# Optimization experiments

Measured on AMD Instinct MI355X. Metric: run time of the kernel, lower is better.

The kernel has to match this reference:

```python
import jax, jax.numpy as jnp
import numpy as np
import math

B, S, D, H = 8, 1024, 1024, 16
DH = D // H  # 64


def setup_inputs() -> dict:
    key = jax.random.key(0)
    ks = jax.random.split(key, 10)
    inputs = jax.random.normal(ks[0], (B, S, D), dtype=jnp.float32)
    mask = jax.random.randint(ks[1], (B, S, S), 0, 2) == 1  # bool [B,S,S]
    sc = 1.0 / math.sqrt(D)
    # per-head projection weights stacked: [H, D, DH], biases [H, DH]
    Wq = jax.random.normal(ks[2], (H, D, DH), dtype=jnp.float32) * sc
    bq = jax.random.normal(ks[3], (H, DH), dtype=jnp.float32) * 0.02
    Wk = jax.random.normal(ks[4], (H, D, DH), dtype=jnp.float32) * sc
    bk = jax.random.normal(ks[5], (H, DH), dtype=jnp.float32) * 0.02
    Wv = jax.random.normal(ks[6], (H, D, DH), dtype=jnp.float32) * sc
    bv = jax.random.normal(ks[7], (H, DH), dtype=jnp.float32) * 0.02
    Wo = jax.random.normal(ks[8], (D, D), dtype=jnp.float32) * sc
    bo = jax.random.normal(ks[9], (D,), dtype=jnp.float32) * 0.02
    return {"inputs": inputs, "mask": mask, "Wq": Wq, "bq": bq, "Wk": Wk,
            "bk": bk, "Wv": Wv, "bv": bv, "Wo": Wo, "bo": bo}


def reference(inputs, mask, Wq, bq, Wk, bk, Wv, bv, Wo, bo):
    d_model = inputs.shape[-1]
    scale = 1.0 / jnp.sqrt(jnp.asarray(d_model, inputs.dtype))  # note: sqrt(d_model), as in source
    # batched per-head projections: [B,H,S,DH]
    Q = jnp.einsum('bsd,hde->bhse', inputs, Wq) + bq[None, :, None, :]
    K = jnp.einsum('bsd,hde->bhse', inputs, Wk) + bk[None, :, None, :]
    V = jnp.einsum('bsd,hde->bhse', inputs, Wv) + bv[None, :, None, :]
    scores = jnp.einsum('bhse,bhte->bhst', Q, K) * scale  # [B,H,S,S]
    scores = jnp.where(mask[:, None, :, :], jnp.asarray(-1e9, scores.dtype), scores)
    attn = jax.nn.softmax(scores, axis=-1)
    ctx = jnp.einsum('bhst,bhte->bhse', attn, V)  # [B,H,S,DH]
    # concat heads along last dim (head h -> slice h*DH:(h+1)*DH), matches torch.cat
    bsz, h, s, dh = ctx.shape
    x = ctx.transpose(0, 2, 1, 3).reshape(bsz, s, h * dh)
    return x @ Wo + bo
```

## Files before the change

kernel.cpp:

```cpp
#include <hip/hip_runtime.h>
#include <hip/hip_bf16.h>
#include <stdint.h>


typedef __attribute__((ext_vector_type(8))) short short8;
typedef __attribute__((ext_vector_type(4))) float floatx4;

__device__ __forceinline__ int swz(int r, int kc) { return r * 8 + (kc ^ (r & 7)); }
__device__ __forceinline__ short8 as_frag(uint4 u) { return __builtin_bit_cast(short8, u); }
__device__ __forceinline__ floatx4 mfma16(short8 a, short8 b, floatx4 c) {
    return __builtin_amdgcn_mfma_f32_16x16x32_bf16(a, b, c, 0, 0, 0);
}
__device__ __forceinline__ unsigned short f2bu(float f) {
    return __builtin_bit_cast(unsigned short, __float2bfloat16(f));
}
__device__ __forceinline__ short f2b(float f) {
    return __builtin_bit_cast(short, __float2bfloat16(f));
}
__device__ __forceinline__ float b2f(short s) {
    return __bfloat162float(__builtin_bit_cast(__hip_bfloat16, s));
}
__device__ __forceinline__ void dma16(const void* g, void* l) {
    __builtin_amdgcn_global_load_lds(
        (const __attribute__((address_space(1))) uint32_t*)g,
        (__attribute__((address_space(3))) uint32_t*)l, 16, 0, 0);
}
__device__ __forceinline__ uint2 pack4(float a, float b, float c, float d) {
    uint2 p;
    p.x = (unsigned)f2bu(a) | ((unsigned)f2bu(b) << 16);
    p.y = (unsigned)f2bu(c) | ((unsigned)f2bu(d) << 16);
    return p;
}

__device__ __forceinline__ void detect_mode(const unsigned* Xw, int* s_is32) {
    if (threadIdx.x < 64) {
        unsigned lo = Xw[threadIdx.x] & 0xFFFFu;
        unsigned e = (lo >> 7) & 0xFFu;
        unsigned long long bal = __ballot(e >= 88u && e <= 150u);
        if (threadIdx.x == 0) *s_is32 = (bal != ~0ull) ? 1 : 0;
    }
    __syncthreads();
}

__device__ __forceinline__ float load_elt(const void* p, size_t idx, int is32) {
    return is32 ? ((const float*)p)[idx]
                : __bfloat162float(((const __hip_bfloat16*)p)[idx]);
}

__global__ __launch_bounds__(256) void prep_all(
    const void* __restrict__ Wq, const void* __restrict__ Wk,
    const void* __restrict__ Wv, const void* __restrict__ Wo,
    const void* __restrict__ bq, const void* __restrict__ bk,
    const void* __restrict__ bv, const void* __restrict__ bo,
    const void* __restrict__ mask_raw, const void* __restrict__ X,
    __hip_bfloat16* __restrict__ WT, __hip_bfloat16* __restrict__ WoT,
    __hip_bfloat16* __restrict__ bc, unsigned long long* __restrict__ bits64,
    __hip_bfloat16* __restrict__ Xb, int do_x)
{
    __shared__ __hip_bfloat16 T[64][72];
    __shared__ int s_is32;
    int blk = blockIdx.x;
    int tid = threadIdx.x;
    const unsigned* Xw = (const unsigned*)X;

    if (blk < 1024) {
        detect_mode(Xw, &s_is32);
        const void* src; size_t src_off;
        __hip_bfloat16* dst;
        int src_ld, dst_ld;
        if (blk < 768) {
            int p = blk >> 8;
            int rem = blk & 255;
            int h = rem >> 4, dt = rem & 15;
            src = (p == 0) ? Wq : (p == 1) ? Wk : Wv;
            src_off = ((size_t)h * 1024 + (size_t)dt * 64) * 64;
            dst = WT + (((size_t)p * 16 + h) * 64) * 1024 + dt * 64;
            src_ld = 64; dst_ld = 1024;
        } else {
            int t = blk - 768;
            int kt = t >> 4, nt = t & 15;
            src = Wo; src_off = (size_t)kt * 64 * 1024 + nt * 64;
            dst = WoT + (size_t)nt * 64 * 1024 + kt * 64;
            src_ld = 1024; dst_ld = 1024;
        }
        #pragma unroll
        for (int i = 0; i < 16; i++) {
            int idx = tid + i * 256;
            int r = idx >> 6, c = idx & 63;
            T[c][r] = __float2bfloat16(load_elt(src, src_off + (size_t)r * src_ld + c, s_is32));
        }
        __syncthreads();
        #pragma unroll
        for (int i = 0; i < 16; i++) {
            int idx = tid + i * 256;
            int r = idx >> 6, c = idx & 63;
            dst[(size_t)r * dst_ld + c] = T[r][c];
        }
    } else if (blk == 1024) {
        detect_mode(Xw, &s_is32);
        #pragma unroll
        for (int i = 0; i < 16; i++) {
            int idx = tid + i * 256;
            int which = idx >> 10, j = idx & 1023;
            const void* src = (which == 0) ? bq : (which == 1) ? bk : (which == 2) ? bv : bo;
            bc[idx] = __float2bfloat16(load_elt(src, j, s_is32));
        }
    } else if (blk < 1537) {
        int blkL = blk - 1025;
        const int* mi = (const int*)mask_raw;
        const unsigned char* mb = (const unsigned char*)mask_raw;
        int lane = tid & 63;
        bool ok = true;
        #pragma unroll
        for (int i = 0; i < 4; i++) {
            unsigned v = (unsigned)mi[lane * 4 + i];
            if (v > 1u) ok = false;
        }
        bool is_i32 = (__ballot(ok) == ~0ull);
        int gw = (blkL * 256 + tid) >> 6;
        const int NW = 512 * 4;
        const int NWORDS = (8 * 1024 * 1024) / 64;
        if (is_i32) {
            for (int i = gw; i < NWORDS; i += NW) {
                int mv = mi[(size_t)i * 64 + lane];
                unsigned long long bal = __ballot(mv != 0);
                if (lane == 0) {
                    int bb = i >> 14, q = (i >> 4) & 1023, t = i & 15;
                    bits64[((size_t)bb << 14) + ((size_t)t << 10) + q] = bal;
                }
            }
        } else {
            for (int i = gw; i < NWORDS; i += NW) {
                int mv = mb[(size_t)i * 64 + lane];
                unsigned long long bal = __ballot(mv != 0);
                if (lane == 0) {
                    int bb = i >> 14, q = (i >> 4) & 1023, t = i & 15;
                    bits64[((size_t)bb << 14) + ((size_t)t << 10) + q] = bal;
                }
            }
        }
    } else if (do_x) {
        detect_mode(Xw, &s_is32);
        int blkL = blk - 1537;
        size_t g = ((size_t)blkL * 256 + tid) * 16;
        if (s_is32) {
            const float* Xf = (const float*)X;
            #pragma unroll
            for (int half = 0; half < 2; half++) {
                float4 f0 = *(const float4*)(Xf + g + half * 8);
                float4 f1 = *(const float4*)(Xf + g + half * 8 + 4);
                short8 s;
                s[0] = f2b(f0.x); s[1] = f2b(f0.y); s[2] = f2b(f0.z); s[3] = f2b(f0.w);
                s[4] = f2b(f1.x); s[5] = f2b(f1.y); s[6] = f2b(f1.z); s[7] = f2b(f1.w);
                *(uint4*)(Xb + g + half * 8) = __builtin_bit_cast(uint4, s);
            }
        } else {
            const uint4* Xu = (const uint4*)X;
            *(uint4*)(Xb + g)     = Xu[g / 8];
            *(uint4*)(Xb + g + 8) = Xu[g / 8 + 1];
        }
    }
}

__global__ __launch_bounds__(256, 2) void qkv_gemm_dma(
    const __hip_bfloat16* __restrict__ Xb,
    const __hip_bfloat16* __restrict__ WT,
    const __hip_bfloat16* __restrict__ bc,
    __hip_bfloat16* __restrict__ Q,
    __hip_bfloat16* __restrict__ Ko,
    __hip_bfloat16* __restrict__ Vt)
{
    __shared__ uint4 AsU[256 * 8];
    __shared__ uint4 BsU[128 * 8];
    int tid = threadIdx.x, lane = tid & 63, wave = tid >> 6;
    int quad = lane >> 4, ln = lane & 15;
    int mw = wave & 1, nw = wave >> 1;
    int m0 = blockIdx.x * 256;
    int n0 = blockIdx.y * 128;
    const __hip_bfloat16* Wp = WT + (size_t)n0 * 1024;

    floatx4 acc[8][4];
    #pragma unroll
    for (int i = 0; i < 8; i++)
        #pragma unroll
        for (int j = 0; j < 4; j++) acc[i][j] = (floatx4){0.f, 0.f, 0.f, 0.f};

    for (int k0 = 0; k0 < 1024; k0 += 64) {
        #pragma unroll
        for (int i = 0; i < 8; i++) {
            int r = wave * 64 + i * 8 + (lane >> 3);
            int kc = (lane & 7) ^ (r & 7);
            char* lds = (char*)AsU + (size_t)(wave * 512 + i * 64) * 16;
            dma16(Xb + (size_t)(m0 + r) * 1024 + k0 + kc * 8, lds);
        }
        #pragma unroll
        for (int i = 0; i < 4; i++) {
            int r = wave * 32 + i * 8 + (lane >> 3);
            int kc = (lane & 7) ^ (r & 7);
            char* lds = (char*)BsU + (size_t)(wave * 256 + i * 64) * 16;
            dma16(Wp + (size_t)r * 1024 + k0 + kc * 8, lds);
        }
        __syncthreads();
        #pragma unroll
        for (int kk = 0; kk < 2; kk++) {
            short8 af[8], bf[4];
            #pragma unroll
            for (int mi = 0; mi < 8; mi++)
                af[mi] = as_frag(AsU[swz(mw * 128 + mi * 16 + ln, kk * 4 + quad)]);
            #pragma unroll
            for (int ni = 0; ni < 4; ni++)
                bf[ni] = as_frag(BsU[swz(nw * 64 + ni * 16 + ln, kk * 4 + quad)]);
            #pragma unroll
            for (int mi = 0; mi < 8; mi++)
                #pragma unroll
                for (int ni = 0; ni < 4; ni++)
                    acc[mi][ni] = mfma16(af[mi], bf[ni], acc[mi][ni]);
        }
        __syncthreads();
    }

    int b = m0 >> 10;
    int s0 = m0 & 1023;
    int proj = n0 >> 10;
    if (proj == 2) {
        #pragma unroll
        for (int ni = 0; ni < 4; ni++) {
            int n = n0 + nw * 64 + ni * 16 + ln;
            int h = (n >> 6) & 15, e = n & 63;
            float bval = __bfloat162float(bc[2 * 1024 + (n & 1023)]);
            #pragma unroll
            for (int mi = 0; mi < 8; mi++) {
                int sb = s0 + mw * 128 + mi * 16 + quad * 4;
                uint2 pk = pack4(acc[mi][ni][0] + bval, acc[mi][ni][1] + bval,
                                 acc[mi][ni][2] + bval, acc[mi][ni][3] + bval);
                *(uint2*)(Vt + (((size_t)b * 16 + h) * 64 + e) * 1024 + sb) = pk;
            }
        }
    } else {
        __hip_bfloat16* P = (proj == 0) ? Q : Ko;
        #pragma unroll
        for (int ni = 0; ni < 4; ni++) {
            int n = n0 + nw * 64 + ni * 16 + ln;
            int h = (n >> 6) & 15, e = n & 63;
            float bval = __bfloat162float(bc[proj * 1024 + (n & 1023)]);
            #pragma unroll
            for (int mi = 0; mi < 8; mi++) {
                #pragma unroll
                for (int r = 0; r < 4; r++) {
                    int s = s0 + mw * 128 + mi * 16 + quad * 4 + r;
                    P[(((size_t)b * 16 + h) * 1024 + s) * 64 + e] =
                        __float2bfloat16(acc[mi][ni][r] + bval);
                }
            }
        }
    }
}

__global__ __launch_bounds__(256) void qkv_gemm2(
    const void* __restrict__ Xsrc,
    const __hip_bfloat16* __restrict__ WT,
    const __hip_bfloat16* __restrict__ bc,
    __hip_bfloat16* __restrict__ Q,
    __hip_bfloat16* __restrict__ Ko,
    __hip_bfloat16* __restrict__ Vt)
{
    __shared__ int s_is32;
    detect_mode((const unsigned*)Xsrc, &s_is32);
    __shared__ uint4 AsU[128 * 8];
    __shared__ uint4 BsU[128 * 8];
    int tid = threadIdx.x, lane = tid & 63, wave = tid >> 6;
    int quad = lane >> 4, ln = lane & 15;
    int m0 = blockIdx.x * 128;
    int n0 = blockIdx.y * 128;
    const __hip_bfloat16* Wp = WT + (size_t)n0 * 1024;
    const float* Xf = (const float*)Xsrc;
    const __hip_bfloat16* Xh = (const __hip_bfloat16*)Xsrc;

    floatx4 acc[2][8];
    #pragma unroll
    for (int i = 0; i < 2; i++)
        #pragma unroll
        for (int j = 0; j < 8; j++) acc[i][j] = (floatx4){0.f, 0.f, 0.f, 0.f};

    for (int k0 = 0; k0 < 1024; k0 += 64) {
        if (s_is32) {
            #pragma unroll
            for (int i = 0; i < 4; i++) {
                int id = tid + i * 256;
                int r = id >> 3, kc = id & 7;
                size_t off = (size_t)(m0 + r) * 1024 + k0 + kc * 8;
                float4 f0 = *(const float4*)(Xf + off);
                float4 f1 = *(const float4*)(Xf + off + 4);
                short8 s;
                s[0] = f2b(f0.x); s[1] = f2b(f0.y); s[2] = f2b(f0.z); s[3] = f2b(f0.w);
                s[4] = f2b(f1.x); s[5] = f2b(f1.y); s[6] = f2b(f1.z); s[7] = f2b(f1.w);
                AsU[swz(r, kc)] = __builtin_bit_cast(uint4, s);
            }
        } else {
            #pragma unroll
            for (int i = 0; i < 4; i++) {
                int id = tid + i * 256;
                int r = id >> 3, kc = id & 7;
                AsU[swz(r, kc)] = *(const uint4*)(Xh + (size_t)(m0 + r) * 1024 + k0 + kc * 8);
            }
        }
        #pragma unroll
        for (int i = 0; i < 4; i++) {
            int id = tid + i * 256;
            int r = id >> 3, kc = id & 7;
            BsU[swz(r, kc)] = *(const uint4*)(Wp + (size_t)r * 1024 + k0 + kc * 8);
        }
        __syncthreads();
        #pragma unroll
        for (int kk = 0; kk < 2; kk++) {
            short8 a0 = as_frag(AsU[swz(wave * 32 + ln, kk * 4 + quad)]);
            short8 a1 = as_frag(AsU[swz(wave * 32 + 16 + ln, kk * 4 + quad)]);
            #pragma unroll
            for (int nt = 0; nt < 8; nt++) {
                short8 bf = as_frag(BsU[swz(nt * 16 + ln, kk * 4 + quad)]);
                acc[0][nt] = mfma16(a0, bf, acc[0][nt]);
                acc[1][nt] = mfma16(a1, bf, acc[1][nt]);
            }
        }
        __syncthreads();
    }

    int b = m0 >> 10;
    int s0 = m0 & 1023;
    #pragma unroll
    for (int nt = 0; nt < 8; nt++) {
        int n = n0 + nt * 16 + ln;
        int proj = n >> 10, h = (n >> 6) & 15, e = n & 63;
        float bval = __bfloat162float(bc[proj * 1024 + (n & 1023)]);
        #pragma unroll
        for (int mt = 0; mt < 2; mt++) {
            #pragma unroll
            for (int r = 0; r < 4; r++) {
                int s = s0 + wave * 32 + mt * 16 + quad * 4 + r;
                float v = acc[mt][nt][r] + bval;
                if (proj == 2) {
                    Vt[(((size_t)b * 16 + h) * 64 + e) * 1024 + s] = __float2bfloat16(v);
                } else {
                    __hip_bfloat16* P = (proj == 0) ? Q : Ko;
                    P[(((size_t)b * 16 + h) * 1024 + s) * 64 + e] = __float2bfloat16(v);
                }
            }
        }
    }
}

__global__ __launch_bounds__(512, 4) void attn(
    const __hip_bfloat16* __restrict__ Q,
    const __hip_bfloat16* __restrict__ K,
    const __hip_bfloat16* __restrict__ Vt,
    const unsigned long long* __restrict__ bits,
    __hip_bfloat16* __restrict__ ctx)
{
    __shared__ uint4 KsU[2 * 512];
    __shared__ uint4 VsU[2 * 512];
    __shared__ uint4 PsU[8 * 256];

    int tid = threadIdx.x, lane = tid & 63, w = tid >> 6;
    int quad = lane >> 4, ln = lane & 15;
    int bh = blockIdx.x;
    int q0 = blockIdx.y * 256;
    int b = bh >> 4, h = bh & 15;
    const __hip_bfloat16* Qp = Q + (size_t)bh * 1024 * 64;
    const __hip_bfloat16* Kp = K + (size_t)bh * 1024 * 64;
    const __hip_bfloat16* Vp = Vt + (size_t)bh * 64 * 1024;
    const unsigned long long* bp = bits + (size_t)b * 16 * 1024;

    short8 qf[2][2];
    #pragma unroll
    for (int g = 0; g < 2; g++)
        #pragma unroll
        for (int kk = 0; kk < 2; kk++)
            qf[g][kk] = as_frag(*(const uint4*)(
                Qp + (size_t)(q0 + w * 32 + g * 16 + ln) * 64 + kk * 32 + quad * 8));

    int r8 = lane >> 3;
    int kc = (lane & 7) ^ r8;

    floatx4 acc_o[2][4];
    #pragma unroll
    for (int g = 0; g < 2; g++)
        #pragma unroll
        for (int i = 0; i < 4; i++) acc_o[g][i] = (floatx4){0.f, 0.f, 0.f, 0.f};
    float lsum[2] = {0.f, 0.f};
    const float C2 = 0.04508422f;
    __hip_bfloat16* Pw = (__hip_bfloat16*)&PsU[w * 256];

    for (int t0 = 0; t0 < 1024; t0 += 128) {
        __syncthreads();
        #pragma unroll
        for (int i = 0; i < 2; i++) {
            int tK = t0 + i * 64 + w * 8 + r8;
            dma16(Kp + (size_t)tK * 64 + kc * 8,
                  (char*)KsU + (size_t)(i * 512 + w * 64) * 16);
            int e = w * 8 + r8;
            dma16(Vp + (size_t)e * 1024 + t0 + i * 64 + kc * 8,
                  (char*)VsU + (size_t)(i * 512 + w * 64) * 16);
        }
        __syncthreads();

        #pragma unroll
        for (int s = 0; s < 2; s++) {
            int t64 = (t0 >> 6) + s;
            unsigned long long mcur0 = bp[((size_t)t64 << 10) + q0 + w * 32 + ln];
            unsigned long long mcur1 = bp[((size_t)t64 << 10) + q0 + w * 32 + 16 + ln];
            const uint4* Ks = KsU + s * 512;
            const uint4* Vs = VsU + s * 512;

            floatx4 st[2][4];
            #pragma unroll
            for (int g = 0; g < 2; g++)
                #pragma unroll
                for (int i = 0; i < 4; i++) st[g][i] = (floatx4){0.f, 0.f, 0.f, 0.f};
            __builtin_amdgcn_s_setprio(1);
            #pragma unroll
            for (int kk = 0; kk < 2; kk++) {
                #pragma unroll
                for (int tt = 0; tt < 4; tt++) {
                    short8 kf = as_frag(Ks[swz(tt * 16 + ln, kk * 4 + quad)]);
                    st[0][tt] = mfma16(kf, qf[0][kk], st[0][tt]);
                    st[1][tt] = mfma16(kf, qf[1][kk], st[1][tt]);
                }
            }
            __builtin_amdgcn_s_setprio(0);

            #pragma unroll
            for (int g = 0; g < 2; g++) {
                int qloc = g * 16 + ln;
                unsigned long long msh = (g ? mcur1 : mcur0) >> (quad * 4);
                #pragma unroll
                for (int tt = 0; tt < 4; tt++) {
                    unsigned mb = (unsigned)(msh >> (tt * 16)) & 0xFu;
                    float pe0 = (mb & 1u) ? 0.f : __builtin_amdgcn_exp2f(st[g][tt][0] * C2);
                    float pe1 = (mb & 2u) ? 0.f : __builtin_amdgcn_exp2f(st[g][tt][1] * C2);
                    float pe2 = (mb & 4u) ? 0.f : __builtin_amdgcn_exp2f(st[g][tt][2] * C2);
                    float pe3 = (mb & 8u) ? 0.f : __builtin_amdgcn_exp2f(st[g][tt][3] * C2);
                    lsum[g] += (pe0 + pe1) + (pe2 + pe3);
                    int kcp = tt * 2 + (quad >> 1);
                    int off = qloc * 64 + (kcp ^ (qloc & 7)) * 8 + (quad & 1) * 4;
                    *(uint2*)(Pw + off) = pack4(pe0, pe1, pe2, pe3);
                }
            }

            __builtin_amdgcn_s_setprio(1);
            #pragma unroll
            for (int kk = 0; kk < 2; kk++) {
                short8 pf0 = as_frag(PsU[w * 256 + swz(0 * 16 + ln, kk * 4 + quad)]);
                short8 pf1 = as_frag(PsU[w * 256 + swz(1 * 16 + ln, kk * 4 + quad)]);
                #pragma unroll
                for (int et = 0; et < 4; et++) {
                    short8 vf = as_frag(Vs[swz(et * 16 + ln, kk * 4 + quad)]);
                    acc_o[0][et] = mfma16(vf, pf0, acc_o[0][et]);
                    acc_o[1][et] = mfma16(vf, pf1, acc_o[1][et]);
                }
            }
            __builtin_amdgcn_s_setprio(0);
        }
    }

    #pragma unroll
    for (int g = 0; g < 2; g++) {
        lsum[g] += __shfl_xor(lsum[g], 16, 64);
        lsum[g] += __shfl_xor(lsum[g], 32, 64);
    }

    #pragma unroll
    for (int g = 0; g < 2; g++) {
        float inv = 1.f / fmaxf(lsum[g], 1e-20f);
        int s = q0 + w * 32 + g * 16 + ln;
        __hip_bfloat16* crow = ctx + ((size_t)b * 1024 + s) * 1024 + h * 64 + quad * 4;
        #pragma unroll
        for (int et = 0; et < 4; et++) {
            uint2 pk = pack4(acc_o[g][et][0] * inv, acc_o[g][et][1] * inv,
                             acc_o[g][et][2] * inv, acc_o[g][et][3] * inv);
            *(uint2*)(crow + et * 16) = pk;
        }
    }
}

__global__ __launch_bounds__(256) void out_gemm_dma(
    const __hip_bfloat16* __restrict__ Cx,
    const __hip_bfloat16* __restrict__ WoT,
    const __hip_bfloat16* __restrict__ bc,
    const unsigned* __restrict__ Xw,
    void* __restrict__ dout,
    int direct)
{
    __shared__ int s_is32;
    detect_mode(Xw, &s_is32);
    __shared__ uint4 AsU[128 * 8];
    __shared__ uint4 BsU[128 * 8];
    int tid = threadIdx.x, lane = tid & 63, wave = tid >> 6;
    int quad = lane >> 4, ln = lane & 15;
    int mw = wave & 1, nw = wave >> 1;
    int m0 = blockIdx.x * 128;
    int n0 = blockIdx.y * 128;

    floatx4 acc[4][4];
    #pragma unroll
    for (int i = 0; i < 4; i++)
        #pragma unroll
        for (int j = 0; j < 4; j++) acc[i][j] = (floatx4){0.f, 0.f, 0.f, 0.f};

    for (int k0 = 0; k0 < 1024; k0 += 64) {
        #pragma unroll
        for (int i = 0; i < 4; i++) {
            int r = wave * 32 + i * 8 + (lane >> 3);
            int kc = (lane & 7) ^ (r & 7);
            char* ldsA = (char*)AsU + (size_t)(wave * 256 + i * 64) * 16;
            char* ldsB = (char*)BsU + (size_t)(wave * 256 + i * 64) * 16;
            dma16(Cx + (size_t)(m0 + r) * 1024 + k0 + kc * 8, ldsA);
            dma16(WoT + (size_t)(n0 + r) * 1024 + k0 + kc * 8, ldsB);
        }
        __syncthreads();
        #pragma unroll
        for (int kk = 0; kk < 2; kk++) {
            short8 af[4], bf[4];
            #pragma unroll
            for (int mi = 0; mi < 4; mi++)
                af[mi] = as_frag(AsU[swz(mw * 64 + mi * 16 + ln, kk * 4 + quad)]);
            #pragma unroll
            for (int ni = 0; ni < 4; ni++)
                bf[ni] = as_frag(BsU[swz(nw * 64 + ni * 16 + ln, kk * 4 + quad)]);
            #pragma unroll
            for (int mi = 0; mi < 4; mi++)
                #pragma unroll
                for (int ni = 0; ni < 4; ni++)
                    acc[mi][ni] = mfma16(af[mi], bf[ni], acc[mi][ni]);
        }
        __syncthreads();
    }

    const __hip_bfloat16* bo = bc + 3 * 1024;
    #pragma unroll
    for (int ni = 0; ni < 4; ni++) {
        int n = n0 + nw * 64 + ni * 16 + ln;
        float bval = __bfloat162float(bo[n]);
        #pragma unroll
        for (int mi = 0; mi < 4; mi++) {
            #pragma unroll
            for (int r = 0; r < 4; r++) {
                int m = m0 + mw * 64 + mi * 16 + quad * 4 + r;
                float v = acc[mi][ni][r] + bval;
                if (direct && s_is32) ((float*)dout)[(size_t)m * 1024 + n] = v;
                else ((__hip_bfloat16*)dout)[(size_t)m * 1024 + n] = __float2bfloat16(v);
            }
        }
    }
}

__global__ __launch_bounds__(256) void emit_out(
    const __hip_bfloat16* __restrict__ Fo, const unsigned* __restrict__ Xw,
    void* __restrict__ dout)
{
    __shared__ int s_is32;
    detect_mode(Xw, &s_is32);
    size_t g = (size_t)blockIdx.x * 256 + threadIdx.x;
    uint4 u = *(const uint4*)(Fo + g * 8);
    if (s_is32) {
        short8 s = __builtin_bit_cast(short8, u);
        float4 f0, f1;
        f0.x = b2f(s[0]); f0.y = b2f(s[1]); f0.z = b2f(s[2]); f0.w = b2f(s[3]);
        f1.x = b2f(s[4]); f1.y = b2f(s[5]); f1.z = b2f(s[6]); f1.w = b2f(s[7]);
        *(float4*)((float*)dout + g * 8) = f0;
        *(float4*)((float*)dout + g * 8 + 4) = f1;
    } else {
        *(uint4*)((__hip_bfloat16*)dout + g * 8) = u;
    }
}

extern "C" void kernel_launch(void* const* d_in, const int* in_sizes, int n_in,
                              void* d_out, int out_size, void* d_ws, size_t ws_size,
                              hipStream_t stream) {
    const void* X  = d_in[0];
    const void* mk = d_in[1];
    const void* Wq = d_in[2];
    const void* bq = d_in[3];
    const void* Wk = d_in[4];
    const void* bk = d_in[5];
    const void* Wv = d_in[6];
    const void* bv = d_in[7];
    const void* Wo = d_in[8];
    const void* bo = d_in[9];
    const unsigned* Xw = (const unsigned*)X;

    char* ws = (char*)d_ws;
    __hip_bfloat16*     WT   = (__hip_bfloat16*)(ws);
    __hip_bfloat16*     WoT  = (__hip_bfloat16*)(ws + ((size_t)6 << 20));
    unsigned long long* bits = (unsigned long long*)(ws + ((size_t)8 << 20));
    __hip_bfloat16*     bc   = (__hip_bfloat16*)(ws + ((size_t)9 << 20));
    __hip_bfloat16*     Xb   = (__hip_bfloat16*)(ws + ((size_t)10 << 20));
    __hip_bfloat16*     Qb   = (__hip_bfloat16*)(ws + ((size_t)26 << 20));
    __hip_bfloat16*     Kb   = (__hip_bfloat16*)(ws + ((size_t)42 << 20));
    __hip_bfloat16*     Vtb  = (__hip_bfloat16*)(ws + ((size_t)58 << 20));

    bool bigws = ws_size >= ((size_t)74 << 20);

    hipLaunchKernelGGL(prep_all, dim3(3585), dim3(256), 0, stream,
                       Wq, Wk, Wv, Wo, bq, bk, bv, bo, mk, X,
                       WT, WoT, bc, bits, Xb, bigws ? 1 : 0);

    if (bigws) {
        __hip_bfloat16* Cx = Xb;
        hipLaunchKernelGGL(qkv_gemm_dma, dim3(32, 24), dim3(256), 0, stream,
                           Xb, WT, bc, Qb, Kb, Vtb);
        hipLaunchKernelGGL(attn, dim3(128, 4), dim3(512), 0, stream,
                           Qb, Kb, Vtb, bits, Cx);
        hipLaunchKernelGGL(out_gemm_dma, dim3(64, 8), dim3(256), 0, stream,
                           Cx, WoT, bc, Xw, d_out, 1);
    } else {
        __hip_bfloat16* Cx = (__hip_bfloat16*)d_out;
        __hip_bfloat16* Fo = Qb;
        hipLaunchKernelGGL(qkv_gemm2, dim3(64, 24), dim3(256), 0, stream,
                           X, WT, bc, Qb, Kb, Vtb);
        hipLaunchKernelGGL(attn, dim3(128, 4), dim3(512), 0, stream,
                           Qb, Kb, Vtb, bits, Cx);
        hipLaunchKernelGGL(out_gemm_dma, dim3(64, 8), dim3(256), 0, stream,
                           Cx, WoT, bc, Xw, (void*)Fo, 0);
        hipLaunchKernelGGL(emit_out, dim3(4096), dim3(256), 0, stream,
                           Fo, Xw, d_out);
    }
}
```

Baseline: 311.0 us.

## Shrink attention tile to 128 queries, 16 rows per wave, 64-key steps

Restructures the attention kernel so each wave handles 16 query rows instead of 32, and each block covers 128 queries instead of 256 while stepping over keys in 64-wide chunks instead of 128. Shared memory and register use drop, launch bounds raise the occupancy target to 8 blocks, and the grid doubles to 1024 blocks. The aim is more parallelism and latency hiding. In exchange, K/V tiles are reused across half as many queries, so K/V traffic doubles, and there are twice as many barriers per unit of work.

```diff
diff --git a/kernel.cpp b/kernel.cpp
--- a/kernel.cpp
+++ b/kernel.cpp
@@ -349,136 +349,105 @@
     }
 }
 
-__global__ __launch_bounds__(512, 4) void attn(
+__global__ __launch_bounds__(512, 8) void attn(
     const __hip_bfloat16* __restrict__ Q,
     const __hip_bfloat16* __restrict__ K,
     const __hip_bfloat16* __restrict__ Vt,
     const unsigned long long* __restrict__ bits,
     __hip_bfloat16* __restrict__ ctx)
 {
-    __shared__ uint4 KsU[2 * 512];
-    __shared__ uint4 VsU[2 * 512];
-    __shared__ uint4 PsU[8 * 256];
+    __shared__ uint4 KsU[512];
+    __shared__ uint4 VsU[512];
+    __shared__ uint4 PsU[8 * 128];
 
     int tid = threadIdx.x, lane = tid & 63, w = tid >> 6;
     int quad = lane >> 4, ln = lane & 15;
     int bh = blockIdx.x;
-    int q0 = blockIdx.y * 256;
+    int q0 = blockIdx.y * 128;
     int b = bh >> 4, h = bh & 15;
     const __hip_bfloat16* Qp = Q + (size_t)bh * 1024 * 64;
     const __hip_bfloat16* Kp = K + (size_t)bh * 1024 * 64;
     const __hip_bfloat16* Vp = Vt + (size_t)bh * 64 * 1024;
     const unsigned long long* bp = bits + (size_t)b * 16 * 1024;
 
-    short8 qf[2][2];
-    #pragma unroll
-    for (int g = 0; g < 2; g++)
-        #pragma unroll
-        for (int kk = 0; kk < 2; kk++)
-            qf[g][kk] = as_frag(*(const uint4*)(
-                Qp + (size_t)(q0 + w * 32 + g * 16 + ln) * 64 + kk * 32 + quad * 8));
+    short8 qf[2];
+    #pragma unroll
+    for (int kk = 0; kk < 2; kk++)
+        qf[kk] = as_frag(*(const uint4*)(
+            Qp + (size_t)(q0 + w * 16 + ln) * 64 + kk * 32 + quad * 8));
 
     int r8 = lane >> 3;
-    int kc = (lane & 7) ^ r8;
-
-    floatx4 acc_o[2][4];
-    #pragma unroll
-    for (int g = 0; g < 2; g++)
-        #pragma unroll
-        for (int i = 0; i < 4; i++) acc_o[g][i] = (floatx4){0.f, 0.f, 0.f, 0.f};
-    float lsum[2] = {0.f, 0.f};
+    int scc = (lane & 7) ^ r8;
+    int srow = w * 8 + r8;
+    char* kdst = (char*)KsU + (size_t)w * 1024;
+    char* vdst = (char*)VsU + (size_t)w * 1024;
+
+    floatx4 acc[4];
+    #pragma unroll
+    for (int i = 0; i < 4; i++) acc[i] = (floatx4){0.f, 0.f, 0.f, 0.f};
+    float lsum = 0.f;
     const float C2 = 0.04508422f;
-    __hip_bfloat16* Pw = (__hip_bfloat16*)&PsU[w * 256];
-
-    for (int t0 = 0; t0 < 1024; t0 += 128) {
-        __syncthreads();
-        #pragma unroll
-        for (int i = 0; i < 2; i++) {
-            int tK = t0 + i * 64 + w * 8 + r8;
-            dma16(Kp + (size_t)tK * 64 + kc * 8,
-                  (char*)KsU + (size_t)(i * 512 + w * 64) * 16);
-            int e = w * 8 + r8;
-            dma16(Vp + (size_t)e * 1024 + t0 + i * 64 + kc * 8,
-                  (char*)VsU + (size_t)(i * 512 + w * 64) * 16);
-        }
-        __syncthreads();
-
-        #pragma unroll
-        for (int s = 0; s < 2; s++) {
-            int t64 = (t0 >> 6) + s;
-            unsigned long long mcur0 = bp[((size_t)t64 << 10) + q0 + w * 32 + ln];
-            unsigned long long mcur1 = bp[((size_t)t64 << 10) + q0 + w * 32 + 16 + ln];
-            const uint4* Ks = KsU + s * 512;
-            const uint4* Vs = VsU + s * 512;
-
-            floatx4 st[2][4];
-            #pragma unroll
-            for (int g = 0; g < 2; g++)
-                #pragma unroll
-                for (int i = 0; i < 4; i++) st[g][i] = (floatx4){0.f, 0.f, 0.f, 0.f};
-            __builtin_amdgcn_s_setprio(1);
-            #pragma unroll
-            for (int kk = 0; kk < 2; kk++) {
-                #pragma unroll
-                for (int tt = 0; tt < 4; tt++) {
-                    short8 kf = as_frag(Ks[swz(tt * 16 + ln, kk * 4 + quad)]);
-                    st[0][tt] = mfma16(kf, qf[0][kk], st[0][tt]);
-                    st[1][tt] = mfma16(kf, qf[1][kk], st[1][tt]);
-                }
-            }
-            __builtin_amdgcn_s_setprio(0);
-
-            #pragma unroll
-            for (int g = 0; g < 2; g++) {
-                int qloc = g * 16 + ln;
-                unsigned long long msh = (g ? mcur1 : mcur0) >> (quad * 4);
-                #pragma unroll
-                for (int tt = 0; tt < 4; tt++) {
-                    unsigned mb = (unsigned)(msh >> (tt * 16)) & 0xFu;
-                    float pe0 = (mb & 1u) ? 0.f : __builtin_amdgcn_exp2f(st[g][tt][0] * C2);
-                    float pe1 = (mb & 2u) ? 0.f : __builtin_amdgcn_exp2f(st[g][tt][1] * C2);
-                    float pe2 = (mb & 4u) ? 0.f : __builtin_amdgcn_exp2f(st[g][tt][2] * C2);
-                    float pe3 = (mb & 8u) ? 0.f : __builtin_amdgcn_exp2f(st[g][tt][3] * C2);
-                    lsum[g] += (pe0 + pe1) + (pe2 + pe3);
-                    int kcp = tt * 2 + (quad >> 1);
-                    int off = qloc * 64 + (kcp ^ (qloc & 7)) * 8 + (quad & 1) * 4;
-                    *(uint2*)(Pw + off) = pack4(pe0, pe1, pe2, pe3);
-                }
-            }
-
-            __builtin_amdgcn_s_setprio(1);
-            #pragma unroll
-            for (int kk = 0; kk < 2; kk++) {
-                short8 pf0 = as_frag(PsU[w * 256 + swz(0 * 16 + ln, kk * 4 + quad)]);
-                short8 pf1 = as_frag(PsU[w * 256 + swz(1 * 16 + ln, kk * 4 + quad)]);
-                #pragma unroll
-                for (int et = 0; et < 4; et++) {
-                    short8 vf = as_frag(Vs[swz(et * 16 + ln, kk * 4 + quad)]);
-                    acc_o[0][et] = mfma16(vf, pf0, acc_o[0][et]);
-                    acc_o[1][et] = mfma16(vf, pf1, acc_o[1][et]);
-                }
-            }
-            __builtin_amdgcn_s_setprio(0);
-        }
-    }
-
-    #pragma unroll
-    for (int g = 0; g < 2; g++) {
-        lsum[g] += __shfl_xor(lsum[g], 16, 64);
-        lsum[g] += __shfl_xor(lsum[g], 32, 64);
-    }
-
-    #pragma unroll
-    for (int g = 0; g < 2; g++) {
-        float inv = 1.f / fmaxf(lsum[g], 1e-20f);
-        int s = q0 + w * 32 + g * 16 + ln;
-        __hip_bfloat16* crow = ctx + ((size_t)b * 1024 + s) * 1024 + h * 64 + quad * 4;
-        #pragma unroll
-        for (int et = 0; et < 4; et++) {
-            uint2 pk = pack4(acc_o[g][et][0] * inv, acc_o[g][et][1] * inv,
-                             acc_o[g][et][2] * inv, acc_o[g][et][3] * inv);
-            *(uint2*)(crow + et * 16) = pk;
-        }
+    __hip_bfloat16* Pw = (__hip_bfloat16*)&PsU[w * 128];
+
+    for (int t0 = 0; t0 < 1024; t0 += 64) {
+        __syncthreads();
+        dma16(Kp + (size_t)(t0 + srow) * 64 + scc * 8, kdst);
+        dma16(Vp + (size_t)srow * 1024 + t0 + scc * 8, vdst);
+        unsigned long long mcur = bp[((size_t)(t0 >> 6) << 10) + q0 + w * 16 + ln];
+        __syncthreads();
+
+        floatx4 st[4];
+        #pragma unroll
+        for (int i = 0; i < 4; i++) st[i] = (floatx4){0.f, 0.f, 0.f, 0.f};
+        __builtin_amdgcn_s_setprio(1);
+        #pragma unroll
+        for (int kk = 0; kk < 2; kk++) {
+            #pragma unroll
+            for (int tt = 0; tt < 4; tt++) {
+                short8 kf = as_frag(KsU[swz(tt * 16 + ln, kk * 4 + quad)]);
+                st[tt] = mfma16(kf, qf[kk], st[tt]);
+            }
+        }
+        __builtin_amdgcn_s_setprio(0);
+
+        unsigned long long msh = mcur >> (quad * 4);
+        #pragma unroll
+        for (int tt = 0; tt < 4; tt++) {
+            unsigned mb = (unsigned)(msh >> (tt * 16)) & 0xFu;
+            float pe0 = (mb & 1u) ? 0.f : __builtin_amdgcn_exp2f(st[tt][0] * C2);
+            float pe1 = (mb & 2u) ? 0.f : __builtin_amdgcn_exp2f(st[tt][1] * C2);
+            float pe2 = (mb & 4u) ? 0.f : __builtin_amdgcn_exp2f(st[tt][2] * C2);
+            float pe3 = (mb & 8u) ? 0.f : __builtin_amdgcn_exp2f(st[tt][3] * C2);
+            lsum += (pe0 + pe1) + (pe2 + pe3);
+            int kcp = tt * 2 + (quad >> 1);
+            int off = ln * 64 + (kcp ^ (ln & 7)) * 8 + (quad & 1) * 4;
+            *(uint2*)(Pw + off) = pack4(pe0, pe1, pe2, pe3);
+        }
+
+        __builtin_amdgcn_s_setprio(1);
+        #pragma unroll
+        for (int kk = 0; kk < 2; kk++) {
+            short8 pf = as_frag(PsU[w * 128 + swz(ln, kk * 4 + quad)]);
+            #pragma unroll
+            for (int et = 0; et < 4; et++) {
+                short8 vf = as_frag(VsU[swz(et * 16 + ln, kk * 4 + quad)]);
+                acc[et] = mfma16(vf, pf, acc[et]);
+            }
+        }
+        __builtin_amdgcn_s_setprio(0);
+    }
+
+    lsum += __shfl_xor(lsum, 16, 64);
+    lsum += __shfl_xor(lsum, 32, 64);
+
+    float inv = 1.f / fmaxf(lsum, 1e-20f);
+    int s = q0 + w * 16 + ln;
+    __hip_bfloat16* crow = ctx + ((size_t)b * 1024 + s) * 1024 + h * 64 + quad * 4;
+    #pragma unroll
+    for (int et = 0; et < 4; et++) {
+        uint2 pk = pack4(acc[et][0] * inv, acc[et][1] * inv,
+                         acc[et][2] * inv, acc[et][3] * inv);
+        *(uint2*)(crow + et * 16) = pk;
     }
 }
 
@@ -608,7 +577,7 @@
         __hip_bfloat16* Cx = Xb;
         hipLaunchKernelGGL(qkv_gemm_dma, dim3(32, 24), dim3(256), 0, stream,
                            Xb, WT, bc, Qb, Kb, Vtb);
-        hipLaunchKernelGGL(attn, dim3(128, 4), dim3(512), 0, stream,
+        hipLaunchKernelGGL(attn, dim3(128, 8), dim3(512), 0, stream,
                            Qb, Kb, Vtb, bits, Cx);
         hipLaunchKernelGGL(out_gemm_dma, dim3(64, 8), dim3(256), 0, stream,
                            Cx, WoT, bc, Xw, d_out, 1);
@@ -617,7 +586,7 @@
         __hip_bfloat16* Fo = Qb;
         hipLaunchKernelGGL(qkv_gemm2, dim3(64, 24), dim3(256), 0, stream,
                            X, WT, bc, Qb, Kb, Vtb);
-        hipLaunchKernelGGL(attn, dim3(128, 4), dim3(512), 0, stream,
+        hipLaunchKernelGGL(attn, dim3(128, 8), dim3(512), 0, stream,
                            Qb, Kb, Vtb, bits, Cx);
         hipLaunchKernelGGL(out_gemm_dma, dim3(64, 8), dim3(256), 0, stream,
                            Cx, WoT, bc, Xw, (void*)Fo, 0);
```

Result: slower. 317.6 us (+2.1%).
